# Optimization experiments

Measured on AMD Instinct MI355X. Metric: run time of the kernel, lower is better.

## Reference

```python
import jax, jax.numpy as jnp
import numpy as np

# Simulates GEMM + intra-node reduce-scatter across `world` ranks on one device.
# Rank r holds A[r]: [M, K_local] and weight[r]: [N, K_local] (K split over ranks).
# Math: reduced = sum_r A[r] @ weight[r]^T  (the all-reduce part),
# then scatter rows: rank r keeps reduced[r*M_per:(r+1)*M_per].

WORLD = 8
M = 8192
N = 2048
K_LOCAL = 256  # K_total = WORLD * K_LOCAL = 2048


def setup_inputs() -> dict:
    key = jax.random.key(0)
    k1, k2 = jax.random.split(key)
    A = jax.random.normal(k1, (WORLD, M, K_LOCAL), dtype=jnp.float32)
    weight = jax.random.normal(k2, (WORLD, N, K_LOCAL), dtype=jnp.float32) * 0.02
    return {"A": A, "weight": weight}


def reference(A, weight):
    world, m, _ = A.shape
    n = weight.shape[1]
    # Fused per-rank GEMM + reduce over ranks: [M, N]
    reduced = jnp.einsum("rmk,rnk->mn", A, weight)
    # Scatter: rank r gets its contiguous M/world row block -> [world, M_per, N]
    m_per = m // world
    return reduced.reshape(world, m_per, n)
```

## Files before the change

kernel.cpp:

```cpp
#include <hip/hip_runtime.h>
#include <hip/hip_bf16.h>

typedef __bf16 bf16x8 __attribute__((ext_vector_type(8)));
typedef __bf16 bf16x4 __attribute__((ext_vector_type(4)));
typedef float f32x4 __attribute__((ext_vector_type(4)));

#define WORLD 8
#define M_DIM 8192
#define N_DIM 2048
#define KL 256
#define K_TOT 2048

#define BM 256
#define BN 256
#define BK 64
#define NT (K_TOT / BK)
#define NITER (NT / 2)

#define AS1 __attribute__((address_space(1)))
#define AS3 __attribute__((address_space(3)))

#define BAR()    __builtin_amdgcn_s_barrier()
#define LGKM0()  do { asm volatile("s_waitcnt lgkmcnt(0)" ::: "memory"); \
                      __builtin_amdgcn_sched_barrier(0); } while (0)
#define VMCNT4() asm volatile("s_waitcnt vmcnt(4)" ::: "memory")
#define PRIO1()  __builtin_amdgcn_s_setprio(1)
#define PRIO0()  __builtin_amdgcn_s_setprio(0)

__global__ __launch_bounds__(256) void GemmRS_convert_kernel(
    const float* __restrict__ A,
    const float* __restrict__ W,
    __bf16* __restrict__ Abf,
    __bf16* __restrict__ Wbf)
{
    const long long GA = (long long)WORLD * M_DIM * KL / 4;
    const long long GW = (long long)WORLD * N_DIM * KL / 4;
    const long long stride = (long long)gridDim.x * blockDim.x;
    for (long long g = (long long)blockIdx.x * blockDim.x + threadIdx.x;
         g < GA + GW; g += stride) {
        if (g < GA) {
            const long long e = g * 4;
            const int k = (int)(e & (KL - 1));
            const int m = (int)((e >> 8) & (M_DIM - 1));
            const int r = (int)(e >> 21);
            const float4 v = *reinterpret_cast<const float4*>(A + e);
            bf16x4 o;
            o[0] = (__bf16)v.x; o[1] = (__bf16)v.y;
            o[2] = (__bf16)v.z; o[3] = (__bf16)v.w;
            *reinterpret_cast<bf16x4*>(Abf + (size_t)m * K_TOT + r * KL + k) = o;
        } else {
            const long long e = (g - GA) * 4;
            const int k = (int)(e & (KL - 1));
            const int n = (int)((e >> 8) & (N_DIM - 1));
            const int r = (int)(e >> 19);
            const float4 v = *reinterpret_cast<const float4*>(W + e);
            bf16x4 o;
            o[0] = (__bf16)v.x; o[1] = (__bf16)v.y;
            o[2] = (__bf16)v.z; o[3] = (__bf16)v.w;
            *reinterpret_cast<bf16x4*>(Wbf + (size_t)n * K_TOT + r * KL + k) = o;
        }
    }
}


__device__ __forceinline__ bf16x8 ldsread(const __bf16* p) {
    bf16x8 r;
    unsigned a = (unsigned)(unsigned long long)
        (const AS3 __bf16*)p;
    asm volatile("ds_read_b128 %0, %1" : "=v"(r) : "v"(a));
    return r;
}

__device__ __forceinline__ void stage_half(const __bf16* srcbase, __bf16* dstbase,
                                           int lane, int wave) {
    const int rl = lane >> 3;
    const int g  = (lane & 7) ^ rl;
    const __bf16* s = srcbase + (size_t)(wave * 8 + rl) * K_TOT + g * 8;
#pragma unroll
    for (int j = 0; j < 2; ++j) {
        __builtin_amdgcn_global_load_lds(
            (const AS1 void*)(s + (size_t)(j * 64) * K_TOT),
            (AS3 void*)(dstbase + (j * 64 + wave * 8) * BK),
            16, 0, 0);
    }
}

template<int MH>
__device__ __forceinline__ void read_A(bf16x8 (&a)[4][2], const __bf16* Lbase,
                                       int arow, int gk0, int gk1) {
#pragma unroll
    for (int f = 0; f < 4; ++f) {
        const __bf16* rp = Lbase + arow + (MH * 4 + f) * 16 * BK;
        a[f][0] = ldsread(rp + gk0);
        a[f][1] = ldsread(rp + gk1);
    }
}

__device__ __forceinline__ void read_B(bf16x8 (&b)[4][2], const __bf16* Lbase,
                                       int brow, int gk0, int gk1) {
#pragma unroll
    for (int f = 0; f < 4; ++f) {
        const __bf16* rp = Lbase + brow + f * 16 * BK;
        b[f][0] = ldsread(rp + gk0);
        b[f][1] = ldsread(rp + gk1);
    }
}

template<int MH, int NH>
__device__ __forceinline__ void mma_quad(f32x4 (&acc)[8][4],
                                         bf16x8 (&a)[4][2], bf16x8 (&b)[4][2]) {
#pragma unroll
    for (int f = 0; f < 4; ++f)
#pragma unroll
        for (int j = 0; j < 2; ++j) {
            f32x4 c = acc[MH * 4 + f][NH * 2 + j];
            c = __builtin_amdgcn_mfma_f32_16x16x32_bf16(a[f][0], b[NH * 2 + j][0], c, 0, 0, 0);
            c = __builtin_amdgcn_mfma_f32_16x16x32_bf16(a[f][1], b[NH * 2 + j][1], c, 0, 0, 0);
            acc[MH * 4 + f][NH * 2 + j] = c;
        }
}

__global__ __launch_bounds__(512, 2) void GemmRS_gemm_kernel(
    const __bf16* __restrict__ Abf,
    const __bf16* __restrict__ Wbf,
    float* __restrict__ C)
{
    __shared__ __bf16 lds[2][2][BM * BK];

    const int tid  = threadIdx.x;
    const int lane = tid & 63;
    const int wave = tid >> 6;
    const int wr   = wave >> 2;
    const int wc   = wave & 3;

    const int bid = blockIdx.x;
    const int swz = (bid & 7) * 32 + (bid >> 3);
    const int tm = swz >> 3;
    const int tn = swz & 7;
    const size_t m0 = (size_t)tm * BM;
    const size_t n0 = (size_t)tn * BN;

    const __bf16* aptr = Abf + m0 * K_TOT;
    const __bf16* bptr = Wbf + n0 * K_TOT;

    __bf16* LA0 = &lds[0][0][0];
    __bf16* LB0 = &lds[0][1][0];
    __bf16* LA1 = &lds[1][0][0];
    __bf16* LB1 = &lds[1][1][0];

    auto ST = [&](__bf16* dst, const __bf16* srcp, int h, int t) {
        stage_half(srcp + (size_t)(h * 128) * K_TOT + t * BK,
                   dst + h * 128 * BK, lane, wave);
    };

    const int r15 = lane & 15;
    const int g2  = lane >> 4;
    const int l7  = lane & 7;
    const int gk0 = ((g2)     ^ l7) * 8;
    const int gk1 = ((4 + g2) ^ l7) * 8;
    const int arow = (wr * 128 + r15) * BK;
    const int brow = (wc * 64  + r15) * BK;

    f32x4 acc[8][4];
#pragma unroll
    for (int i = 0; i < 8; ++i)
#pragma unroll
        for (int j = 0; j < 4; ++j)
            acc[i][j] = (f32x4){0.f, 0.f, 0.f, 0.f};

    bf16x8 a[4][2], b[4][2];

    ST(LA0, aptr, 0, 0);
    ST(LA0, aptr, 1, 0);
    ST(LB0, bptr, 0, 0);
    ST(LB0, bptr, 1, 0);
    ST(LB1, bptr, 0, 1);
    ST(LB1, bptr, 1, 1);
    VMCNT4();
    BAR();

    for (int i = 0; i < NITER; ++i) {
        const int t1 = 2 * i + 1;
        const int t2 = (2 * i + 2 < NT) ? 2 * i + 2 : NT - 1;
        const int t3 = (2 * i + 3 < NT) ? 2 * i + 3 : NT - 1;

        read_A<0>(a, LA0, arow, gk0, gk1);
        read_B(b, LB0, brow, gk0, gk1);
        ST(LA1, aptr, 0, t1);
        BAR(); LGKM0();
        PRIO1(); mma_quad<0, 0>(acc, a, b); PRIO0();
        BAR();
        ST(LA1, aptr, 1, t1);
        BAR(); LGKM0();
        PRIO1(); mma_quad<0, 1>(acc, a, b); PRIO0();
        BAR();
        read_A<1>(a, LA0, arow, gk0, gk1);
        ST(LB0, bptr, 0, t2);
        BAR(); LGKM0();
        PRIO1(); mma_quad<1, 1>(acc, a, b); PRIO0();
        BAR();
        ST(LB0, bptr, 1, t2);
        BAR(); LGKM0();
        PRIO1(); mma_quad<1, 0>(acc, a, b); PRIO0();
        VMCNT4();
        BAR();

        read_A<0>(a, LA1, arow, gk0, gk1);
        read_B(b, LB1, brow, gk0, gk1);
        ST(LA0, aptr, 0, t2);
        BAR(); LGKM0();
        PRIO1(); mma_quad<0, 0>(acc, a, b); PRIO0();
        BAR();
        ST(LA0, aptr, 1, t2);
        BAR(); LGKM0();
        PRIO1(); mma_quad<0, 1>(acc, a, b); PRIO0();
        BAR();
        read_A<1>(a, LA1, arow, gk0, gk1);
        ST(LB1, bptr, 0, t3);
        BAR(); LGKM0();
        PRIO1(); mma_quad<1, 1>(acc, a, b); PRIO0();
        BAR();
        ST(LB1, bptr, 1, t3);
        BAR(); LGKM0();
        PRIO1(); mma_quad<1, 0>(acc, a, b); PRIO0();
        VMCNT4();
        BAR();
    }

#pragma unroll
    for (int fa = 0; fa < 8; ++fa)
#pragma unroll
        for (int fb = 0; fb < 4; ++fb) {
            float* cp = C + (m0 + wr * 128 + fa * 16 + g2 * 4) * (size_t)N_DIM
                          + n0 + wc * 64 + fb * 16 + r15;
#pragma unroll
            for (int q = 0; q < 4; ++q)
                cp[(size_t)q * N_DIM] = acc[fa][fb][q];
        }
}

extern "C" void kernel_launch(void* const* d_in, const int* in_sizes, int n_in,
                              void* d_out, int out_size, void* d_ws, size_t ws_size,
                              hipStream_t stream) {
    (void)in_sizes; (void)n_in; (void)out_size; (void)ws_size;
    const float* A = (const float*)d_in[0];
    const float* W = (const float*)d_in[1];
    float* C = (float*)d_out;

    __bf16* Abf = (__bf16*)d_ws;
    __bf16* Wbf = (__bf16*)((char*)d_ws + (size_t)M_DIM * K_TOT * 2);

    GemmRS_convert_kernel<<<2048, 256, 0, stream>>>(A, W, Abf, Wbf);
    GemmRS_gemm_kernel<<<(M_DIM / BM) * (N_DIM / BN), 512, 0, stream>>>(Abf, Wbf, C);
}
```

Before: 83.28 us.

## Relax LDS waitcounts in GEMM main loop and stage epilogue through LDS

Splits the B fragment reads so the first MFMA quad waits only until part of the LDS reads have landed (lgkmcnt(4) instead of 0), and drops the wait before the last quad since no new LDS reads were issued. The epilogue now transposes each 16-row accumulator block through a per-wave LDS scratch area, so global stores become 16-byte vector writes along N instead of scalar strided stores. This risks incorrect ordering if the lgkmcnt counts don't match the issued read order, and the epilogue reuses the LDS tile buffer with no barrier between per-wave write and read, relying on wave-local access.

```diff
diff --git a/kernel.cpp b/kernel.cpp
--- a/kernel.cpp
+++ b/kernel.cpp
@@ -21,7 +21,7 @@
 #define AS3 __attribute__((address_space(3)))
 
 #define BAR()    __builtin_amdgcn_s_barrier()
-#define LGKM0()  do { asm volatile("s_waitcnt lgkmcnt(0)" ::: "memory"); \
+#define LGKMC(n) do { asm volatile("s_waitcnt lgkmcnt(" #n ")" ::: "memory"); \
                       __builtin_amdgcn_sched_barrier(0); } while (0)
 #define VMCNT4() asm volatile("s_waitcnt vmcnt(4)" ::: "memory")
 #define PRIO1()  __builtin_amdgcn_s_setprio(1)
@@ -65,8 +65,7 @@
 
 __device__ __forceinline__ bf16x8 ldsread(const __bf16* p) {
     bf16x8 r;
-    unsigned a = (unsigned)(unsigned long long)
-        (const AS3 __bf16*)p;
+    unsigned a = (unsigned)(unsigned long long)(const AS3 __bf16*)p;
     asm volatile("ds_read_b128 %0, %1" : "=v"(r) : "v"(a));
     return r;
 }
@@ -96,10 +95,11 @@
     }
 }
 
+template<int F0, int F1>
 __device__ __forceinline__ void read_B(bf16x8 (&b)[4][2], const __bf16* Lbase,
                                        int brow, int gk0, int gk1) {
 #pragma unroll
-    for (int f = 0; f < 4; ++f) {
+    for (int f = F0; f < F1; ++f) {
         const __bf16* rp = Lbase + brow + f * 16 * BK;
         b[f][0] = ldsread(rp + gk0);
         b[f][1] = ldsread(rp + gk1);
@@ -185,58 +185,67 @@
         const int t3 = (2 * i + 3 < NT) ? 2 * i + 3 : NT - 1;
 
         read_A<0>(a, LA0, arow, gk0, gk1);
-        read_B(b, LB0, brow, gk0, gk1);
+        read_B<0, 2>(b, LB0, brow, gk0, gk1);
+        read_B<2, 4>(b, LB0, brow, gk0, gk1);
         ST(LA1, aptr, 0, t1);
-        BAR(); LGKM0();
+        BAR(); LGKMC(4);
         PRIO1(); mma_quad<0, 0>(acc, a, b); PRIO0();
         BAR();
         ST(LA1, aptr, 1, t1);
-        BAR(); LGKM0();
+        BAR(); LGKMC(0);
         PRIO1(); mma_quad<0, 1>(acc, a, b); PRIO0();
         BAR();
         read_A<1>(a, LA0, arow, gk0, gk1);
         ST(LB0, bptr, 0, t2);
-        BAR(); LGKM0();
+        BAR(); LGKMC(0);
         PRIO1(); mma_quad<1, 1>(acc, a, b); PRIO0();
         BAR();
         ST(LB0, bptr, 1, t2);
-        BAR(); LGKM0();
+        BAR();
         PRIO1(); mma_quad<1, 0>(acc, a, b); PRIO0();
         VMCNT4();
         BAR();
 
         read_A<0>(a, LA1, arow, gk0, gk1);
-        read_B(b, LB1, brow, gk0, gk1);
+        read_B<0, 2>(b, LB1, brow, gk0, gk1);
+        read_B<2, 4>(b, LB1, brow, gk0, gk1);
         ST(LA0, aptr, 0, t2);
-        BAR(); LGKM0();
+        BAR(); LGKMC(4);
         PRIO1(); mma_quad<0, 0>(acc, a, b); PRIO0();
         BAR();
         ST(LA0, aptr, 1, t2);
-        BAR(); LGKM0();
+        BAR(); LGKMC(0);
         PRIO1(); mma_quad<0, 1>(acc, a, b); PRIO0();
         BAR();
         read_A<1>(a, LA1, arow, gk0, gk1);
         ST(LB1, bptr, 0, t3);
-        BAR(); LGKM0();
+        BAR(); LGKMC(0);
         PRIO1(); mma_quad<1, 1>(acc, a, b); PRIO0();
         BAR();
         ST(LB1, bptr, 1, t3);
-        BAR(); LGKM0();
+        BAR();
         PRIO1(); mma_quad<1, 0>(acc, a, b); PRIO0();
         VMCNT4();
         BAR();
     }
 
-#pragma unroll
-    for (int fa = 0; fa < 8; ++fa)
-#pragma unroll
-        for (int fb = 0; fb < 4; ++fb) {
-            float* cp = C + (m0 + wr * 128 + fa * 16 + g2 * 4) * (size_t)N_DIM
-                          + n0 + wc * 64 + fb * 16 + r15;
+    float* eb = reinterpret_cast<float*>(&lds[0][0][0]) + wave * 1088;
+#pragma unroll
+    for (int fa = 0; fa < 8; ++fa) {
+#pragma unroll
+        for (int fb = 0; fb < 4; ++fb)
 #pragma unroll
             for (int q = 0; q < 4; ++q)
-                cp[(size_t)q * N_DIM] = acc[fa][fb][q];
+                eb[(g2 * 4 + q) * 68 + fb * 16 + r15] = acc[fa][fb][q];
+#pragma unroll
+        for (int j = 0; j < 4; ++j) {
+            const int row = j * 4 + g2;
+            f32x4 v = *reinterpret_cast<const f32x4*>(eb + row * 68 + r15 * 4);
+            *reinterpret_cast<f32x4*>(
+                C + (m0 + wr * 128 + fa * 16 + row) * (size_t)N_DIM
+                  + n0 + wc * 64 + r15 * 4) = v;
         }
+    }
 }
 
 extern "C" void kernel_launch(void* const* d_in, const int* in_sizes, int n_in,
```

After: 87.62 us. 1.05x slower.
